# Performance work log

Measured on AMD Instinct MI355X. Metric: run time of the kernel, lower is better.

The kernel has to match this reference:

```python
import jax, jax.numpy as jnp
import numpy as np

N_NODES = 50000
DEG = 16
N_HEAD = 4
F_IN = 32
F_OUT = 32


def setup_inputs() -> dict:
    key = jax.random.key(0)
    k_h, k_w, k_fw, k_fb = jax.random.split(key, 4)
    h = jax.random.normal(k_h, (N_NODES, F_IN), dtype=jnp.float32)
    # structured edge list: each node has DEG distinct out-neighbors
    src = jnp.repeat(jnp.arange(N_NODES, dtype=jnp.int64), DEG)          # [E]
    offs = (jnp.arange(DEG, dtype=jnp.int64) + 1) * 97                   # distinct offsets
    dst = (src.reshape(N_NODES, DEG) + offs[None, :]).reshape(-1) % N_NODES
    edge_index = jnp.stack([src, dst], axis=0)                           # [2, E]
    # params (xavier-ish init for w, small fc, zero bias)
    gain = 1.414
    bound_w = gain * np.sqrt(6.0 / (F_IN + F_OUT))
    w = jax.random.uniform(k_w, (N_HEAD, F_IN, F_OUT), jnp.float32, -bound_w, bound_w)
    bound_fc = np.sqrt(1.0 / (2 * F_OUT))
    fc_w = jax.random.uniform(k_fw, (1, 2 * F_OUT), jnp.float32, -bound_fc, bound_fc)
    fc_b = jax.random.uniform(k_fb, (1,), jnp.float32, -bound_fc, bound_fc)
    bias = jnp.zeros((F_OUT,), jnp.float32)
    return {"h": h, "edge_index": edge_index, "w": w, "fc_w": fc_w, "fc_b": fc_b, "bias": bias}


def reference(h, edge_index, w, fc_w, fc_b, bias):
    n_head, f_in, f_out = w.shape
    n = h.shape[0]
    src, dst = edge_index[0], edge_index[1]
    hp = jnp.einsum('nf,hfo->hno', h, w)                  # [H, N, F_out]
    # fc([h_src || h_dst]) decomposes into two per-node projections
    w_src = fc_w[0, :f_out]                               # [F_out]
    w_dst = fc_w[0, f_out:]
    a_src = jnp.einsum('hnf,f->hn', hp, w_src)            # [H, N]
    a_dst = jnp.einsum('hnf,f->hn', hp, w_dst)
    e = a_src[:, src] + a_dst[:, dst] + fc_b[0]           # [H, E]
    e = jax.nn.leaky_relu(e, negative_slope=0.2)
    # segment softmax over each source node's neighbor set
    seg_max = jax.ops.segment_max(e.T, src, num_segments=n)   # [N, H]
    e = jnp.exp(e - seg_max.T[:, src])
    seg_sum = jax.ops.segment_sum(e.T, src, num_segments=n)   # [N, H]
    att = e / seg_sum.T[:, src]                                # [H, E]
    # aggregate: out[h, i] = sum_{j in N(i)} att * hp[h, j]  (== adj @ hp)
    msg = att[:, :, None] * hp[:, dst, :]                      # [H, E, F_out]
    agg = jax.vmap(lambda m: jax.ops.segment_sum(m, src, num_segments=n))(msg)  # [H, N, F_out]
    out = agg.mean(axis=0) + bias                              # [N, F_out]
    return out
```

## Files before the change

### kernel.cpp

```cpp
#include <hip/hip_runtime.h>
#include <hip/hip_fp16.h>

#define N_HEAD 4
#define F_IN   32
#define F_OUT  32
#define DEG    16

union H4 { ushort4 u; __half h[4]; };

__device__ __forceinline__ float4 fma4(float a, float4 x, float4 acc) {
    acc.x = fmaf(a, x.x, acc.x);
    acc.y = fmaf(a, x.y, acc.y);
    acc.z = fmaf(a, x.z, acc.z);
    acc.w = fmaf(a, x.w, acc.w);
    return acc;
}

__device__ __forceinline__ float4 shflxor4(float4 v, int m) {
    float4 r;
    r.x = __shfl_xor(v.x, m, 64);
    r.y = __shfl_xor(v.y, m, 64);
    r.z = __shfl_xor(v.z, m, 64);
    r.w = __shfl_xor(v.w, m, 64);
    return r;
}

__global__ __launch_bounds__(256) void gat_proj(
    const float* __restrict__ h, const float* __restrict__ w,
    const float* __restrict__ fc_w,
    ushort4* __restrict__ hp, float* __restrict__ asrc, float* __restrict__ adst,
    int N)
{
    __shared__ float4 wlds[N_HEAD * F_IN * F_OUT / 4];
    int t = threadIdx.x;
    const float4* w4g = (const float4*)w;
    wlds[t]       = w4g[t];
    wlds[t + 256] = w4g[t + 256];
    wlds[t + 512] = w4g[t + 512];
    wlds[t + 768] = w4g[t + 768];
    __syncthreads();

    int wid  = t >> 6;
    int lane = t & 63;
    int p    = lane >> 5;
    int sub  = lane & 31;
    int hh   = sub >> 3;
    int q    = sub & 7;
    int node0 = blockIdx.x * 32;
    int base  = node0 + wid * 8 + p * 4;
    bool full = (node0 + 32 <= N);

    float4 acc[4];
    #pragma unroll
    for (int m = 0; m < 4; ++m) acc[m] = make_float4(0.f, 0.f, 0.f, 0.f);

    const float4* h4 = (const float4*)h;
    if (full) {
        #pragma unroll
        for (int c = 0; c < 8; ++c) {
            float4 wv0 = wlds[hh * 256 + (4 * c + 0) * 8 + q];
            float4 wv1 = wlds[hh * 256 + (4 * c + 1) * 8 + q];
            float4 wv2 = wlds[hh * 256 + (4 * c + 2) * 8 + q];
            float4 wv3 = wlds[hh * 256 + (4 * c + 3) * 8 + q];
            #pragma unroll
            for (int m = 0; m < 4; ++m) {
                float4 hv = h4[(size_t)(base + m) * 8 + c];
                acc[m] = fma4(hv.x, wv0, acc[m]);
                acc[m] = fma4(hv.y, wv1, acc[m]);
                acc[m] = fma4(hv.z, wv2, acc[m]);
                acc[m] = fma4(hv.w, wv3, acc[m]);
            }
        }
    } else {
        #pragma unroll
        for (int c = 0; c < 8; ++c) {
            float4 wv0 = wlds[hh * 256 + (4 * c + 0) * 8 + q];
            float4 wv1 = wlds[hh * 256 + (4 * c + 1) * 8 + q];
            float4 wv2 = wlds[hh * 256 + (4 * c + 2) * 8 + q];
            float4 wv3 = wlds[hh * 256 + (4 * c + 3) * 8 + q];
            #pragma unroll
            for (int m = 0; m < 4; ++m) {
                int node = base + m;
                int nc   = node < N ? node : N - 1;
                float4 hv = h4[(size_t)nc * 8 + c];
                acc[m] = fma4(hv.x, wv0, acc[m]);
                acc[m] = fma4(hv.y, wv1, acc[m]);
                acc[m] = fma4(hv.z, wv2, acc[m]);
                acc[m] = fma4(hv.w, wv3, acc[m]);
            }
        }
    }

    float4 fs4 = ((const float4*)fc_w)[q];
    float4 fd4 = ((const float4*)fc_w)[8 + q];
    float ps[4], pd[4];
    #pragma unroll
    for (int m = 0; m < 4; ++m) {
        ps[m] = acc[m].x * fs4.x + acc[m].y * fs4.y + acc[m].z * fs4.z + acc[m].w * fs4.w;
        pd[m] = acc[m].x * fd4.x + acc[m].y * fd4.y + acc[m].z * fd4.z + acc[m].w * fd4.w;
    }
    #pragma unroll
    for (int msk = 1; msk <= 4; msk <<= 1) {
        #pragma unroll
        for (int m = 0; m < 4; ++m) {
            ps[m] += __shfl_xor(ps[m], msk, 64);
            pd[m] += __shfl_xor(pd[m], msk, 64);
        }
    }

    #pragma unroll
    for (int m = 0; m < 4; ++m) {
        int node = base + m;
        if (full || node < N) {
            H4 pk;
            pk.h[0] = __float2half_rn(acc[m].x);
            pk.h[1] = __float2half_rn(acc[m].y);
            pk.h[2] = __float2half_rn(acc[m].z);
            pk.h[3] = __float2half_rn(acc[m].w);
            hp[(size_t)node * 32 + hh * 8 + q] = pk.u;
            if (q == 0) {
                asrc[node * N_HEAD + hh] = ps[m];
                adst[node * N_HEAD + hh] = pd[m];
            }
        }
    }
}

__global__ __launch_bounds__(256) void gat_agg(
    const int* __restrict__ dst, const ushort4* __restrict__ hp,
    const float* __restrict__ asrc, const float* __restrict__ adst,
    const float* __restrict__ fc_b, const float* __restrict__ bias,
    float* __restrict__ out, int N)
{
    int wave = (int)((blockIdx.x * 256 + threadIdx.x) >> 6);
    int lane = threadIdx.x & 63;
    if (wave >= N) return;
    int node = wave;
    int e2 = lane >> 5;
    int sub = lane & 31;
    int hh = sub >> 3;
    int q  = sub & 7;

    const int4* dr4 = (const int4*)(dst + (size_t)node * DEG);
    int4 d0 = dr4[0], d1 = dr4[1], d2 = dr4[2], d3 = dr4[3];
    int dk[16] = { d0.x, d0.y, d0.z, d0.w, d1.x, d1.y, d1.z, d1.w,
                   d2.x, d2.y, d2.z, d2.w, d3.x, d3.y, d3.z, d3.w };

    float as = asrc[node * N_HEAD + hh];
    float b  = fc_b[0];

    float e[16];
    #pragma unroll
    for (int k = 0; k < 16; ++k) {
        float ad = adst[dk[k] * N_HEAD + hh];
        float v  = as + ad + b;
        e[k] = v > 0.f ? v : 0.2f * v;
    }
    float mx = e[0];
    #pragma unroll
    for (int k = 1; k < 16; ++k) mx = fmaxf(mx, e[k]);
    float s = 0.f;
    #pragma unroll
    for (int k = 0; k < 16; ++k) { e[k] = __expf(e[k] - mx); s += e[k]; }
    float inv = 1.0f / s;

    float4 acc = make_float4(0.f, 0.f, 0.f, 0.f);
    #pragma unroll
    for (int i = 0; i < 8; ++i) {
        int   dki = e2 ? dk[2 * i + 1] : dk[2 * i];
        float p   = e2 ? e[2 * i + 1] : e[2 * i];
        H4 pk;
        pk.u = hp[(size_t)dki * 32 + hh * 8 + q];
        float4 v = make_float4(__half2float(pk.h[0]), __half2float(pk.h[1]),
                               __half2float(pk.h[2]), __half2float(pk.h[3]));
        acc = fma4(p, v, acc);
    }
    acc.x *= inv; acc.y *= inv; acc.z *= inv; acc.w *= inv;

    float4 r;
    r = shflxor4(acc, 32); acc.x += r.x; acc.y += r.y; acc.z += r.z; acc.w += r.w;
    r = shflxor4(acc, 8);  acc.x += r.x; acc.y += r.y; acc.z += r.z; acc.w += r.w;
    r = shflxor4(acc, 16); acc.x += r.x; acc.y += r.y; acc.z += r.z; acc.w += r.w;

    if (lane < 8) {
        float4 b4 = ((const float4*)bias)[q];
        float4 o4;
        o4.x = 0.25f * acc.x + b4.x;
        o4.y = 0.25f * acc.y + b4.y;
        o4.z = 0.25f * acc.z + b4.z;
        o4.w = 0.25f * acc.w + b4.w;
        ((float4*)out)[(size_t)node * 8 + q] = o4;
    }
}

extern "C" void kernel_launch(void* const* d_in, const int* in_sizes, int n_in,
                              void* d_out, int out_size, void* d_ws, size_t ws_size,
                              hipStream_t stream) {
    const float* h    = (const float*)d_in[0];
    const int*   eidx = (const int*)  d_in[1];
    const float* w    = (const float*)d_in[2];
    const float* fc_w = (const float*)d_in[3];
    const float* fc_b = (const float*)d_in[4];
    const float* bias = (const float*)d_in[5];

    int N = in_sizes[0] / F_IN;
    int E = in_sizes[1] / 2;
    const int* dst = eidx + E;

    ushort4* hp  = (ushort4*)d_ws;
    float* asrc  = (float*)(hp + (size_t)N * 32);
    float* adst  = asrc + (size_t)N * N_HEAD;
    float* out   = (float*)d_out;

    gat_proj<<<(N + 31) / 32, 256, 0, stream>>>(h, w, fc_w, hp, asrc, adst, N);
    gat_agg <<<(N + 3) / 4,   256, 0, stream>>>(dst, hp, asrc, adst, fc_b, bias, out, N);
}
```

Before: 108.4 us.

## Process four nodes per wave in aggregation with 16-byte gathers and XCD-aware block remap

The aggregation kernel now gives each wavefront four nodes, 16 lanes per node. Each lane gathers a uint4 of eight fp16 values for all 16 neighbors, replacing ushort4 loads split across two half-waves. Block indices are remapped so consecutive virtual blocks land on the same XCD chunk, which is meant to improve L2 locality for neighbor gathers. The aim is more bytes per load and fewer wasted lanes. The trade-off is more redundant softmax work per lane and more registers.

Measured after the change: 102.4 us. 1.06x faster.

```diff
diff --git a/kernel.cpp b/kernel.cpp
--- a/kernel.cpp
+++ b/kernel.cpp
@@ -7,6 +7,7 @@
 #define DEG    16
 
 union H4 { ushort4 u; __half h[4]; };
+union H8 { uint4 u; __half h[8]; };
 
 __device__ __forceinline__ float4 fma4(float a, float4 x, float4 acc) {
     acc.x = fmaf(a, x.x, acc.x);
@@ -14,15 +15,6 @@
     acc.z = fmaf(a, x.z, acc.z);
     acc.w = fmaf(a, x.w, acc.w);
     return acc;
-}
-
-__device__ __forceinline__ float4 shflxor4(float4 v, int m) {
-    float4 r;
-    r.x = __shfl_xor(v.x, m, 64);
-    r.y = __shfl_xor(v.y, m, 64);
-    r.z = __shfl_xor(v.z, m, 64);
-    r.w = __shfl_xor(v.w, m, 64);
-    return r;
 }
 
 __global__ __launch_bounds__(256) void gat_proj(
@@ -127,69 +119,74 @@
 }
 
 __global__ __launch_bounds__(256) void gat_agg(
-    const int* __restrict__ dst, const ushort4* __restrict__ hp,
+    const int* __restrict__ dst, const uint4* __restrict__ hp,
     const float* __restrict__ asrc, const float* __restrict__ adst,
     const float* __restrict__ fc_b, const float* __restrict__ bias,
     float* __restrict__ out, int N)
 {
-    int wave = (int)((blockIdx.x * 256 + threadIdx.x) >> 6);
-    int lane = threadIdx.x & 63;
-    if (wave >= N) return;
-    int node = wave;
-    int e2 = lane >> 5;
-    int sub = lane & 31;
-    int hh = sub >> 3;
-    int q  = sub & 7;
-
-    const int4* dr4 = (const int4*)(dst + (size_t)node * DEG);
-    int4 d0 = dr4[0], d1 = dr4[1], d2 = dr4[2], d3 = dr4[3];
-    int dk[16] = { d0.x, d0.y, d0.z, d0.w, d1.x, d1.y, d1.z, d1.w,
-                   d2.x, d2.y, d2.z, d2.w, d3.x, d3.y, d3.z, d3.w };
-
-    float as = asrc[node * N_HEAD + hh];
-    float b  = fc_b[0];
-
-    float e[16];
+    int chunk = gridDim.x >> 3;
+    int b  = blockIdx.x;
+    int vb = (b & 7) * chunk + (b >> 3);
+    int t = threadIdx.x;
+    int wid = t >> 6, lane = t & 63;
+    int g = lane >> 4, r = lane & 15;
+    int node  = vb * 16 + wid * 4 + g;
+    int nodec = node < N ? node : N - 1;
+    int c = r >> 2;
+
+    int dk[16];
+    #pragma unroll
+    for (int k = 0; k < 16; ++k) dk[k] = dst[nodec * DEG + k];
+
+    float as = asrc[nodec * N_HEAD + c];
+    float bb = fc_b[0];
+
+    float p[16];
+    float mx = -1e30f;
     #pragma unroll
     for (int k = 0; k < 16; ++k) {
-        float ad = adst[dk[k] * N_HEAD + hh];
-        float v  = as + ad + b;
-        e[k] = v > 0.f ? v : 0.2f * v;
-    }
-    float mx = e[0];
-    #pragma unroll
-    for (int k = 1; k < 16; ++k) mx = fmaxf(mx, e[k]);
+        float v = as + adst[dk[k] * N_HEAD + c] + bb;
+        v = v > 0.f ? v : 0.2f * v;
+        p[k] = v;
+        mx = fmaxf(mx, v);
+    }
     float s = 0.f;
     #pragma unroll
-    for (int k = 0; k < 16; ++k) { e[k] = __expf(e[k] - mx); s += e[k]; }
-    float inv = 1.0f / s;
-
-    float4 acc = make_float4(0.f, 0.f, 0.f, 0.f);
-    #pragma unroll
-    for (int i = 0; i < 8; ++i) {
-        int   dki = e2 ? dk[2 * i + 1] : dk[2 * i];
-        float p   = e2 ? e[2 * i + 1] : e[2 * i];
-        H4 pk;
-        pk.u = hp[(size_t)dki * 32 + hh * 8 + q];
-        float4 v = make_float4(__half2float(pk.h[0]), __half2float(pk.h[1]),
-                               __half2float(pk.h[2]), __half2float(pk.h[3]));
-        acc = fma4(p, v, acc);
-    }
-    acc.x *= inv; acc.y *= inv; acc.z *= inv; acc.w *= inv;
-
-    float4 r;
-    r = shflxor4(acc, 32); acc.x += r.x; acc.y += r.y; acc.z += r.z; acc.w += r.w;
-    r = shflxor4(acc, 8);  acc.x += r.x; acc.y += r.y; acc.z += r.z; acc.w += r.w;
-    r = shflxor4(acc, 16); acc.x += r.x; acc.y += r.y; acc.z += r.z; acc.w += r.w;
-
-    if (lane < 8) {
-        float4 b4 = ((const float4*)bias)[q];
-        float4 o4;
-        o4.x = 0.25f * acc.x + b4.x;
-        o4.y = 0.25f * acc.y + b4.y;
-        o4.z = 0.25f * acc.z + b4.z;
-        o4.w = 0.25f * acc.w + b4.w;
-        ((float4*)out)[(size_t)node * 8 + q] = o4;
+    for (int k = 0; k < 16; ++k) { p[k] = __expf(p[k] - mx); s += p[k]; }
+    float inv = 1.f / s;
+
+    float acc[8];
+    #pragma unroll
+    for (int j = 0; j < 8; ++j) acc[j] = 0.f;
+    #pragma unroll
+    for (int k = 0; k < 16; ++k) {
+        H8 v; v.u = hp[(size_t)dk[k] * 16 + r];
+        float a = p[k];
+        #pragma unroll
+        for (int j = 0; j < 8; ++j) acc[j] = fmaf(a, __half2float(v.h[j]), acc[j]);
+    }
+    #pragma unroll
+    for (int j = 0; j < 8; ++j) acc[j] *= inv;
+
+    #pragma unroll
+    for (int j = 0; j < 8; ++j) acc[j] += __shfl_xor(acc[j], 4, 64);
+    #pragma unroll
+    for (int j = 0; j < 8; ++j) acc[j] += __shfl_xor(acc[j], 8, 64);
+
+    if (node < N && r < 4) {
+        float4 b0 = ((const float4*)bias)[r * 2];
+        float4 b1 = ((const float4*)bias)[r * 2 + 1];
+        float4 o0, o1;
+        o0.x = 0.25f * acc[0] + b0.x;
+        o0.y = 0.25f * acc[1] + b0.y;
+        o0.z = 0.25f * acc[2] + b0.z;
+        o0.w = 0.25f * acc[3] + b0.w;
+        o1.x = 0.25f * acc[4] + b1.x;
+        o1.y = 0.25f * acc[5] + b1.y;
+        o1.z = 0.25f * acc[6] + b1.z;
+        o1.w = 0.25f * acc[7] + b1.w;
+        ((float4*)out)[(size_t)node * 8 + r * 2]     = o0;
+        ((float4*)out)[(size_t)node * 8 + r * 2 + 1] = o1;
     }
 }
 
@@ -213,5 +210,9 @@
     float* out   = (float*)d_out;
 
     gat_proj<<<(N + 31) / 32, 256, 0, stream>>>(h, w, fc_w, hp, asrc, adst, N);
-    gat_agg <<<(N + 3) / 4,   256, 0, stream>>>(dst, hp, asrc, adst, fc_b, bias, out, N);
-}
+
+    int nvb   = (N + 15) / 16;
+    int chunk = (nvb + 7) / 8;
+    gat_agg<<<8 * chunk, 256, 0, stream>>>(dst, (const uint4*)hp, asrc, adst,
+                                           fc_b, bias, out, N);
+}
```
